# Optimization experiments

Hardware: AMD Instinct MI355X
Metric: run time of the kernel (lower is better)

## Reference

```python
import jax, jax.numpy as jnp
import numpy as np

B, C_IN, C_OUT, N, K = 1, 64, 64, 50000, 20


def setup_inputs() -> dict:
    key = jax.random.key(0)
    k1, k2, k3, k4, k5 = jax.random.split(key, 5)
    x = jax.random.normal(k1, (B, C_IN, N, 1), dtype=jnp.float32)
    edge_index = jax.random.randint(k2, (2, B, N, K), 0, N, dtype=jnp.int64)
    dis = jax.random.uniform(k3, (B, N, K), dtype=jnp.float32)
    W = jax.random.normal(k4, (C_OUT, 2 * C_IN), dtype=jnp.float32) * (2.0 / (2 * C_IN)) ** 0.5
    b = jnp.zeros((C_OUT,), dtype=jnp.float32)
    att_w = jax.random.normal(k5, (K,), dtype=jnp.float32) * (2.0 / K) ** 0.5
    att_b = jnp.zeros((1,), dtype=jnp.float32)
    return {"x": x, "edge_index": edge_index, "dis": dis, "W": W, "b": b,
            "att_w": att_w, "att_b": att_b}


def reference(x, edge_index, dis, W, b, att_w, att_b):
    # x: [B, C, N, 1]; edge_index: [2, B, N, K]; dis: [B, N, K]
    x2 = x[..., 0]  # [B, C, N]
    gather = jax.vmap(lambda xb, ib: xb[:, ib])  # per-batch: [C,N] idx[N,K] -> [C,N,K]
    x_i = gather(x2, edge_index[1])  # [B, C, N, K]
    x_j = gather(x2, edge_index[0])  # [B, C, N, K]
    feat = jnp.concatenate([x_i, x_j - x_i], axis=1)  # [B, 2C, N, K]
    # 1x1 conv == channel contraction
    feat = jax.nn.relu(jnp.einsum('oc,bcnk->bonk', W, feat) + b[None, :, None, None])
    # attention over the k channel of dis -> per-node scaler
    scaler = jnp.tanh(jnp.einsum('k,bnk->bn', att_w, dis) + att_b) + 1.0  # [B, N]
    suppression = 2.0 * jax.nn.sigmoid(-dis * scaler[:, :, None])  # [B, N, K]
    feat = feat * suppression[:, None, :, :]  # [B, C_out, N, K]
    return jnp.max(feat, axis=-1, keepdims=True)  # [B, C_out, N, 1]
```

## Files before the change

kernel.cpp:

```cpp
#include <hip/hip_runtime.h>

#define NN 50000
#define KK 20

__device__ __align__(256) ushort g_pool[2][2][NN * 32];
__device__ __align__(256) float  g_sup[NN * KK];

static __device__ __forceinline__ ushort f2bf(float f) {
    unsigned int u = __float_as_uint(f);
    unsigned int r = (u + 0x7FFFu + ((u >> 16) & 1u)) >> 16;
    return (ushort)r;
}
static __device__ __forceinline__ float bfl(unsigned int u) {
    return __uint_as_float(u << 16);
}
static __device__ __forceinline__ float bfh(unsigned int u) {
    return __uint_as_float(u & 0xffff0000u);
}

__global__ __launch_bounds__(256) void prep_kernel(
    const float* __restrict__ x,
    const float* __restrict__ W,
    const float* __restrict__ b,
    const float* __restrict__ dis,
    const float* __restrict__ att_w,
    const float* __restrict__ att_b)
{
    __shared__ float At[64][66];
    __shared__ float Bt[64][66];
    __shared__ float xt[64][132];
    __shared__ float disL[128 * KK];
    __shared__ float scalerL[128];

    const int t  = threadIdx.x;
    const int n0 = blockIdx.x * 128;

    for (int i = t; i < 64 * 64; i += 256) {
        int c = i >> 6, ci = i & 63;
        float w1 = W[c * 128 + ci];
        float w2 = W[c * 128 + 64 + ci];
        At[ci][c] = w1 - w2;
        Bt[ci][c] = w2;
    }
    {
        const int q  = t & 31;
        const int cb = t >> 5;
        const float4* x4 = (const float4*)x;
        const int nq = (n0 >> 2) + q;
        #pragma unroll
        for (int i = 0; i < 8; i++) {
            const int ci = cb * 8 + i;
            float4 v = (nq < 12500) ? x4[ci * 12500 + nq]
                                    : float4{0.f, 0.f, 0.f, 0.f};
            *(float4*)&xt[ci][q * 4] = v;
        }
    }
    for (int i = t; i < 128 * KK; i += 256) {
        const int gi = n0 * KK + i;
        disL[i] = (gi < NN * KK) ? dis[gi] : 0.f;
    }
    __syncthreads();

    if (t < 128) {
        float z = att_b[0];
        #pragma unroll
        for (int k = 0; k < KK; k++) z += att_w[k] * disL[t * KK + k];
        scalerL[t] = 2.f / (1.f + __expf(-2.f * z));
    }
    __syncthreads();

    for (int i = t; i < 128 * KK; i += 256) {
        const int gi = n0 * KK + i;
        if (gi < NN * KK)
            g_sup[gi] = 2.f / (1.f + __expf(disL[i] * scalerL[i / KK]));
    }

    const int c2 = t & 31;
    const int g  = t >> 5;

    float aA0[16], aA1[16], aB0[16], aB1[16];
    #pragma unroll
    for (int j = 0; j < 16; j++) { aA0[j]=0.f; aA1[j]=0.f; aB0[j]=0.f; aB1[j]=0.f; }

    for (int ci = 0; ci < 64; ci++) {
        const float2 a  = *(const float2*)&At[ci][c2 * 2];
        const float2 w2 = *(const float2*)&Bt[ci][c2 * 2];
        const float4* xr = (const float4*)&xt[ci][g * 16];
        #pragma unroll
        for (int q = 0; q < 4; q++) {
            float4 xv = xr[q];
            aA0[q*4+0] += a.x*xv.x;  aA1[q*4+0] += a.y*xv.x;
            aB0[q*4+0] += w2.x*xv.x; aB1[q*4+0] += w2.y*xv.x;
            aA0[q*4+1] += a.x*xv.y;  aA1[q*4+1] += a.y*xv.y;
            aB0[q*4+1] += w2.x*xv.y; aB1[q*4+1] += w2.y*xv.y;
            aA0[q*4+2] += a.x*xv.z;  aA1[q*4+2] += a.y*xv.z;
            aB0[q*4+2] += w2.x*xv.z; aB1[q*4+2] += w2.y*xv.z;
            aA0[q*4+3] += a.x*xv.w;  aA1[q*4+3] += a.y*xv.w;
            aB0[q*4+3] += w2.x*xv.w; aB1[q*4+3] += w2.y*xv.w;
        }
    }

    const float b0 = b[c2 * 2], b1 = b[c2 * 2 + 1];
    const int h  = c2 >> 4;
    const int pp = c2 & 15;
    unsigned int* pool32 = (unsigned int*)g_pool;
    const size_t baseA = (size_t)(h * 2 + 0) * NN * 16;
    const size_t baseB = (size_t)(h * 2 + 1) * NN * 16;
    #pragma unroll
    for (int j = 0; j < 16; j++) {
        const int n = n0 + g * 16 + j;
        if (n < NN) {
            pool32[baseA + (size_t)n * 16 + pp] =
                (unsigned int)f2bf(aA0[j] + b0) | ((unsigned int)f2bf(aA1[j] + b1) << 16);
            pool32[baseB + (size_t)n * 16 + pp] =
                (unsigned int)f2bf(aB0[j]) | ((unsigned int)f2bf(aB1[j]) << 16);
        }
    }
}

__global__ __launch_bounds__(256) void edge_kernel(
    const int* __restrict__ ej,
    const int* __restrict__ ei,
    float* __restrict__ out)
{
    __shared__ float tile[16][36];

    const int t    = threadIdx.x;
    const int lane = t & 63;
    const int w    = t >> 6;
    const int g    = lane >> 3;
    const int q    = lane & 7;
    const int bx   = blockIdx.x;
    const int h    = (bx >= 3125) ? 1 : 0;
    const int n0   = (bx - h * 3125) * 16;
    const int nb   = n0 + w * 4;

    const char* pA = (const char*)&g_pool[h][0][0];
    const char* pB = (const char*)&g_pool[h][1][0];

    int offI[4], offJ[4]; float sup4[4];
    #pragma unroll
    for (int s = 0; s < 4; s++) {
        const int n = nb + s;
        int ii = 0, jj = 0; float sp = 0.f;
        if (lane < KK) {
            ii = __builtin_nontemporal_load(&ei[n * KK + lane]);
            jj = __builtin_nontemporal_load(&ej[n * KK + lane]);
            sp = __builtin_nontemporal_load(&g_sup[n * KK + lane]);
        }
        offI[s] = ii << 6;
        offJ[s] = jj << 6;
        sup4[s] = sp;
    }

    #pragma unroll
    for (int s = 0; s < 4; s++) {
        float4 m = {0.f, 0.f, 0.f, 0.f};
        #pragma unroll
        for (int r = 0; r < 3; r++) {
            const int   src = r * 8 + g;
            const int   oi  = __shfl(offI[s], src);
            const int   oj  = __shfl(offJ[s], src);
            const float sp  = __shfl(sup4[s], src);
            const uint2 a   = *(const uint2*)(pA + oi + q * 8);
            const uint2 bb  = *(const uint2*)(pB + oj + q * 8);
            float v;
            v = fmaxf(bfl(a.x) + bfl(bb.x), 0.f) * sp;  m.x = fmaxf(m.x, v);
            v = fmaxf(bfh(a.x) + bfh(bb.x), 0.f) * sp;  m.y = fmaxf(m.y, v);
            v = fmaxf(bfl(a.y) + bfl(bb.y), 0.f) * sp;  m.z = fmaxf(m.z, v);
            v = fmaxf(bfh(a.y) + bfh(bb.y), 0.f) * sp;  m.w = fmaxf(m.w, v);
        }
        #pragma unroll
        for (int mask = 8; mask <= 32; mask <<= 1) {
            m.x = fmaxf(m.x, __shfl_xor(m.x, mask));
            m.y = fmaxf(m.y, __shfl_xor(m.y, mask));
            m.z = fmaxf(m.z, __shfl_xor(m.z, mask));
            m.w = fmaxf(m.w, __shfl_xor(m.w, mask));
        }
        if (g == 0) *(float4*)&tile[w * 4 + s][q * 4] = m;
    }
    __syncthreads();

    #pragma unroll
    for (int it = 0; it < 2; it++) {
        const int c  = it * 16 + (t >> 4);
        const int nl = t & 15;
        __builtin_nontemporal_store(tile[nl][c],
                                    &out[(size_t)(h * 32 + c) * NN + n0 + nl]);
    }
}

extern "C" void kernel_launch(void* const* d_in, const int* in_sizes, int n_in,
                              void* d_out, int out_size, void* d_ws, size_t ws_size,
                              hipStream_t stream) {
    const float* x     = (const float*)d_in[0];
    const int*   e     = (const int*)d_in[1];
    const float* dis   = (const float*)d_in[2];
    const float* W     = (const float*)d_in[3];
    const float* b     = (const float*)d_in[4];
    const float* att_w = (const float*)d_in[5];
    const float* att_b = (const float*)d_in[6];
    float* out = (float*)d_out;

    (void)d_ws; (void)ws_size;

    prep_kernel<<<(NN + 127) / 128, 256, 0, stream>>>(x, W, b, dis, att_w, att_b);
    edge_kernel<<<2 * 3125, 256, 0, stream>>>(e, e + NN * KK, out);
}
```

Before: 144.6 us.

## Store full 64-channel rows per node and process all channels per block

```diff
diff --git a/kernel.cpp b/kernel.cpp
--- a/kernel.cpp
+++ b/kernel.cpp
@@ -3,7 +3,8 @@
 #define NN 50000
 #define KK 20
 
-__device__ __align__(256) ushort g_pool[2][2][NN * 32];
+__device__ __align__(256) ushort g_poolA[NN * 64];
+__device__ __align__(256) ushort g_poolB[NN * 64];
 __device__ __align__(256) float  g_sup[NN * KK];
 
 static __device__ __forceinline__ ushort f2bf(float f) {
@@ -101,19 +102,16 @@
     }
 
     const float b0 = b[c2 * 2], b1 = b[c2 * 2 + 1];
-    const int h  = c2 >> 4;
-    const int pp = c2 & 15;
-    unsigned int* pool32 = (unsigned int*)g_pool;
-    const size_t baseA = (size_t)(h * 2 + 0) * NN * 16;
-    const size_t baseB = (size_t)(h * 2 + 1) * NN * 16;
+    unsigned int* yA32 = (unsigned int*)g_poolA;
+    unsigned int* yB32 = (unsigned int*)g_poolB;
     #pragma unroll
     for (int j = 0; j < 16; j++) {
         const int n = n0 + g * 16 + j;
         if (n < NN) {
-            pool32[baseA + (size_t)n * 16 + pp] =
-                (unsigned int)f2bf(aA0[j] + b0) | ((unsigned int)f2bf(aA1[j] + b1) << 16);
-            pool32[baseB + (size_t)n * 16 + pp] =
-                (unsigned int)f2bf(aB0[j]) | ((unsigned int)f2bf(aB1[j]) << 16);
+            yA32[n * 32 + c2] = (unsigned int)f2bf(aA0[j] + b0)
+                              | ((unsigned int)f2bf(aA1[j] + b1) << 16);
+            yB32[n * 32 + c2] = (unsigned int)f2bf(aB0[j])
+                              | ((unsigned int)f2bf(aB1[j]) << 16);
         }
     }
 }
@@ -123,20 +121,18 @@
     const int* __restrict__ ei,
     float* __restrict__ out)
 {
-    __shared__ float tile[16][36];
+    __shared__ float tile[16][68];
 
     const int t    = threadIdx.x;
     const int lane = t & 63;
     const int w    = t >> 6;
-    const int g    = lane >> 3;
-    const int q    = lane & 7;
-    const int bx   = blockIdx.x;
-    const int h    = (bx >= 3125) ? 1 : 0;
-    const int n0   = (bx - h * 3125) * 16;
+    const int g    = lane >> 4;
+    const int l    = lane & 15;
+    const int n0   = blockIdx.x * 16;
     const int nb   = n0 + w * 4;
 
-    const char* pA = (const char*)&g_pool[h][0][0];
-    const char* pB = (const char*)&g_pool[h][1][0];
+    const char* pA = (const char*)g_poolA;
+    const char* pB = (const char*)g_poolB;
 
     int offI[4], offJ[4]; float sup4[4];
     #pragma unroll
@@ -148,8 +144,8 @@
             jj = __builtin_nontemporal_load(&ej[n * KK + lane]);
             sp = __builtin_nontemporal_load(&g_sup[n * KK + lane]);
         }
-        offI[s] = ii << 6;
-        offJ[s] = jj << 6;
+        offI[s] = ii << 7;
+        offJ[s] = jj << 7;
         sup4[s] = sp;
     }
 
@@ -157,13 +153,13 @@
     for (int s = 0; s < 4; s++) {
         float4 m = {0.f, 0.f, 0.f, 0.f};
         #pragma unroll
-        for (int r = 0; r < 3; r++) {
-            const int   src = r * 8 + g;
+        for (int kb = 0; kb < 5; kb++) {
+            const int   src = kb * 4 + g;
             const int   oi  = __shfl(offI[s], src);
             const int   oj  = __shfl(offJ[s], src);
             const float sp  = __shfl(sup4[s], src);
-            const uint2 a   = *(const uint2*)(pA + oi + q * 8);
-            const uint2 bb  = *(const uint2*)(pB + oj + q * 8);
+            const uint2 a   = *(const uint2*)(pA + oi + l * 8);
+            const uint2 bb  = *(const uint2*)(pB + oj + l * 8);
             float v;
             v = fmaxf(bfl(a.x) + bfl(bb.x), 0.f) * sp;  m.x = fmaxf(m.x, v);
             v = fmaxf(bfh(a.x) + bfh(bb.x), 0.f) * sp;  m.y = fmaxf(m.y, v);
@@ -171,22 +167,22 @@
             v = fmaxf(bfh(a.y) + bfh(bb.y), 0.f) * sp;  m.w = fmaxf(m.w, v);
         }
         #pragma unroll
-        for (int mask = 8; mask <= 32; mask <<= 1) {
+        for (int mask = 16; mask <= 32; mask <<= 1) {
             m.x = fmaxf(m.x, __shfl_xor(m.x, mask));
             m.y = fmaxf(m.y, __shfl_xor(m.y, mask));
             m.z = fmaxf(m.z, __shfl_xor(m.z, mask));
             m.w = fmaxf(m.w, __shfl_xor(m.w, mask));
         }
-        if (g == 0) *(float4*)&tile[w * 4 + s][q * 4] = m;
+        if (g == 0) *(float4*)&tile[w * 4 + s][l * 4] = m;
     }
     __syncthreads();
 
     #pragma unroll
-    for (int it = 0; it < 2; it++) {
+    for (int it = 0; it < 4; it++) {
         const int c  = it * 16 + (t >> 4);
         const int nl = t & 15;
         __builtin_nontemporal_store(tile[nl][c],
-                                    &out[(size_t)(h * 32 + c) * NN + n0 + nl]);
+                                    &out[(size_t)c * NN + n0 + nl]);
     }
 }
 
@@ -205,5 +201,5 @@
     (void)d_ws; (void)ws_size;
 
     prep_kernel<<<(NN + 127) / 128, 256, 0, stream>>>(x, W, b, dis, att_w, att_b);
-    edge_kernel<<<2 * 3125, 256, 0, stream>>>(e, e + NN * KK, out);
-}
+    edge_kernel<<<NN / 16, 256, 0, stream>>>(e, e + NN * KK, out);
+}
```

Result: faster. 133.5 us (-7.7%).

## Process 40 nodes per edge block and interleave channel halves across blocks

Applied to the files above, without the earlier changes.

```diff
diff --git a/kernel.cpp b/kernel.cpp
--- a/kernel.cpp
+++ b/kernel.cpp
@@ -101,19 +101,19 @@
     }
 
     const float b0 = b[c2 * 2], b1 = b[c2 * 2 + 1];
-    const int h  = c2 >> 4;
+    const int gq = c2 >> 4;
     const int pp = c2 & 15;
-    unsigned int* pool32 = (unsigned int*)g_pool;
-    const size_t baseA = (size_t)(h * 2 + 0) * NN * 16;
-    const size_t baseB = (size_t)(h * 2 + 1) * NN * 16;
+    unsigned int* poolU = (unsigned int*)g_pool;
+    const size_t pa = (size_t)(gq * 2 + 0) * NN * 16;
+    const size_t pb = (size_t)(gq * 2 + 1) * NN * 16;
     #pragma unroll
     for (int j = 0; j < 16; j++) {
         const int n = n0 + g * 16 + j;
         if (n < NN) {
-            pool32[baseA + (size_t)n * 16 + pp] =
-                (unsigned int)f2bf(aA0[j] + b0) | ((unsigned int)f2bf(aA1[j] + b1) << 16);
-            pool32[baseB + (size_t)n * 16 + pp] =
-                (unsigned int)f2bf(aB0[j]) | ((unsigned int)f2bf(aB1[j]) << 16);
+            poolU[pa + (size_t)n * 16 + pp] = (unsigned int)f2bf(aA0[j] + b0)
+                                            | ((unsigned int)f2bf(aA1[j] + b1) << 16);
+            poolU[pb + (size_t)n * 16 + pp] = (unsigned int)f2bf(aB0[j])
+                                            | ((unsigned int)f2bf(aB1[j]) << 16);
         }
     }
 }
@@ -123,24 +123,24 @@
     const int* __restrict__ ei,
     float* __restrict__ out)
 {
-    __shared__ float tile[16][36];
+    __shared__ float tile[40][36];
 
     const int t    = threadIdx.x;
     const int lane = t & 63;
     const int w    = t >> 6;
-    const int g    = lane >> 3;
+    const int slot = lane >> 3;
     const int q    = lane & 7;
     const int bx   = blockIdx.x;
-    const int h    = (bx >= 3125) ? 1 : 0;
-    const int n0   = (bx - h * 3125) * 16;
-    const int nb   = n0 + w * 4;
-
-    const char* pA = (const char*)&g_pool[h][0][0];
-    const char* pB = (const char*)&g_pool[h][1][0];
-
-    int offI[4], offJ[4]; float sup4[4];
-    #pragma unroll
-    for (int s = 0; s < 4; s++) {
+    const int grp  = bx & 1;
+    const int n0   = (bx >> 1) * 40;
+    const int nb   = n0 + w * 10;
+
+    const char* pA = (const char*)&g_pool[grp][0][0];
+    const char* pB = (const char*)&g_pool[grp][1][0];
+
+    int offI[10], offJ[10]; float sup10[10];
+    #pragma unroll
+    for (int s = 0; s < 10; s++) {
         const int n = nb + s;
         int ii = 0, jj = 0; float sp = 0.f;
         if (lane < KK) {
@@ -150,25 +150,24 @@
         }
         offI[s] = ii << 6;
         offJ[s] = jj << 6;
-        sup4[s] = sp;
-    }
-
-    #pragma unroll
-    for (int s = 0; s < 4; s++) {
+        sup10[s] = sp;
+    }
+
+    #pragma unroll
+    for (int s = 0; s < 10; s++) {
         float4 m = {0.f, 0.f, 0.f, 0.f};
         #pragma unroll
         for (int r = 0; r < 3; r++) {
-            const int   src = r * 8 + g;
+            const int   src = r * 8 + slot;
             const int   oi  = __shfl(offI[s], src);
             const int   oj  = __shfl(offJ[s], src);
-            const float sp  = __shfl(sup4[s], src);
+            const float sp  = __shfl(sup10[s], src);
             const uint2 a   = *(const uint2*)(pA + oi + q * 8);
             const uint2 bb  = *(const uint2*)(pB + oj + q * 8);
-            float v;
-            v = fmaxf(bfl(a.x) + bfl(bb.x), 0.f) * sp;  m.x = fmaxf(m.x, v);
-            v = fmaxf(bfh(a.x) + bfh(bb.x), 0.f) * sp;  m.y = fmaxf(m.y, v);
-            v = fmaxf(bfl(a.y) + bfl(bb.y), 0.f) * sp;  m.z = fmaxf(m.z, v);
-            v = fmaxf(bfh(a.y) + bfh(bb.y), 0.f) * sp;  m.w = fmaxf(m.w, v);
+            m.x = fmaxf(m.x, (bfl(a.x) + bfl(bb.x)) * sp);
+            m.y = fmaxf(m.y, (bfh(a.x) + bfh(bb.x)) * sp);
+            m.z = fmaxf(m.z, (bfl(a.y) + bfl(bb.y)) * sp);
+            m.w = fmaxf(m.w, (bfh(a.y) + bfh(bb.y)) * sp);
         }
         #pragma unroll
         for (int mask = 8; mask <= 32; mask <<= 1) {
@@ -177,16 +176,16 @@
             m.z = fmaxf(m.z, __shfl_xor(m.z, mask));
             m.w = fmaxf(m.w, __shfl_xor(m.w, mask));
         }
-        if (g == 0) *(float4*)&tile[w * 4 + s][q * 4] = m;
+        if (slot == 0) *(float4*)&tile[w * 10 + s][q * 4] = m;
     }
     __syncthreads();
 
     #pragma unroll
-    for (int it = 0; it < 2; it++) {
-        const int c  = it * 16 + (t >> 4);
-        const int nl = t & 15;
+    for (int cn = 0; cn < 5; cn++) {
+        const int c  = t >> 3;
+        const int nl = cn * 8 + (t & 7);
         __builtin_nontemporal_store(tile[nl][c],
-                                    &out[(size_t)(h * 32 + c) * NN + n0 + nl]);
+                                    &out[(size_t)(grp * 32 + c) * NN + n0 + nl]);
     }
 }
 
@@ -205,5 +204,5 @@
     (void)d_ws; (void)ws_size;
 
     prep_kernel<<<(NN + 127) / 128, 256, 0, stream>>>(x, W, b, dis, att_w, att_b);
-    edge_kernel<<<2 * 3125, 256, 0, stream>>>(e, e + NN * KK, out);
-}
+    edge_kernel<<<2 * (NN / 40), 256, 0, stream>>>(e, e + NN * KK, out);
+}
```

New measurement: 145.9 us. No clear change (+0.9%).
